# Optimization experiments

Hardware: AMD Instinct MI355X
Metric: run time of the kernel (lower is better)

## Reference

```python
import jax, jax.numpy as jnp
import numpy as np

B_SZ, L_SEQ = 8, 4096
D_MODEL, D_CONV, D_MAMBA = 512, 256, 256
DSTATE, N_HEADS, K, FFN = 64, 4, 3, 2048
EPS = 1e-6


def setup_inputs() -> dict:
    key = jax.random.key(0)
    ks = jax.random.split(key, 14)
    def rn(k, shape, scale=0.02):
        return jax.random.normal(k, shape, jnp.float32) * scale
    return {
        "x": rn(ks[0], (B_SZ, L_SEQ, D_MODEL), 1.0),
        "velocity": rn(ks[1], (B_SZ, L_SEQ, D_MODEL), 0.1),
        "pre_norm_w": jnp.ones((D_MODEL,), jnp.float32),
        "conv_in_w": rn(ks[2], (D_MODEL, 2 * D_CONV)),
        "conv_dw_w": rn(ks[3], (D_CONV, K), 0.1),
        "conv_dw_b": jnp.zeros((D_CONV,), jnp.float32),
        "x_proj_w": rn(ks[4], (D_MODEL, D_MAMBA)),
        "dt_w": rn(ks[5], (D_MODEL, D_MAMBA), 0.001),
        "dt_b": jnp.full((D_MAMBA,), -4.0, jnp.float32),
        "B_w": rn(ks[6], (D_MODEL, DSTATE)),
        "C_w": rn(ks[7], (D_MODEL, DSTATE)),
        "A_log": jnp.tile(jnp.log(jnp.arange(1, DSTATE + 1, dtype=jnp.float32))[None, :], (N_HEADS, 1)),
        "D": jnp.ones((D_MAMBA,), jnp.float32),
        "ssm_out_w": rn(ks[8], (D_MAMBA, D_MAMBA)),
        "out_proj_w": rn(ks[9], (D_MODEL, D_MODEL)),
        "log_beta": jnp.asarray(0.0, jnp.float32),  # sigmoid(0)=0.5 = beta_init
        "ffn_norm_w": jnp.ones((D_MODEL,), jnp.float32),
        "w1": rn(ks[10], (D_MODEL, FFN)),
        "w3": rn(ks[11], (D_MODEL, FFN)),
        "w2": rn(ks[12], (FFN, D_MODEL)),
    }


def _rmsnorm(x, w):
    xf = x.astype(jnp.float32)
    r = jax.lax.rsqrt(jnp.mean(xf * xf, axis=-1, keepdims=True) + EPS)
    return (xf * r).astype(x.dtype) * w


def _gated_conv(xn, conv_in_w, conv_dw_w, conv_dw_b):
    # project to 2*d_conv, causal depthwise conv on first half, silu-gate with second half
    uv = xn @ conv_in_w                       # [B,L,2*dc]
    u, g = uv[..., :D_CONV], uv[..., D_CONV:]
    up = jnp.pad(u, ((0, 0), (K - 1, 0), (0, 0)))
    L = xn.shape[1]
    conv = conv_dw_b
    for k in range(K):                        # tiny fixed kernel loop
        conv = conv + up[:, k:k + L, :] * conv_dw_w[:, k]
    return conv * jax.nn.silu(g)              # [B,L,d_conv]


def _ssm(xn, x_proj_w, dt_w, dt_b, B_w, C_w, A_log, D, ssm_out_w):
    x_ssm = xn @ x_proj_w                                     # [B,L,dm]
    dt_raw = jnp.clip(xn @ dt_w + dt_b, -10.0, 5.0)
    dt = jnp.clip(jax.nn.softplus(dt_raw), 1e-4, 0.1)         # [B,L,dm]
    Bm = xn @ B_w                                             # [B,L,ds]
    Cm = xn @ C_w
    Bm = Bm / jnp.clip(jnp.linalg.norm(Bm, axis=-1, keepdims=True), 1.0)
    Cm = Cm / jnp.clip(jnp.linalg.norm(Cm, axis=-1, keepdims=True), 1.0)
    A = -jnp.exp(A_log.reshape(-1))                           # [dm], channel c -> head c//ds, state c%ds
    Bfull = jnp.tile(Bm, (1, 1, N_HEADS))                     # [B,L,dm]: B[..., c % ds]
    Cfull = jnp.tile(Cm, (1, 1, N_HEADS))
    decay = jnp.exp(dt * A)                                   # [B,L,dm]
    inp = dt * Bfull * x_ssm

    def step(h, di):
        d_, i_ = di
        h = d_ * h + i_
        return h, h

    h0 = jnp.zeros((xn.shape[0], D_MAMBA), x_ssm.dtype)
    _, hs = jax.lax.scan(step, h0, (jnp.swapaxes(decay, 0, 1), jnp.swapaxes(inp, 0, 1)))
    y = jnp.swapaxes(hs, 0, 1) * Cfull + D * x_ssm            # [B,L,dm]
    return y @ ssm_out_w


def reference(x, velocity, pre_norm_w, conv_in_w, conv_dw_w, conv_dw_b,
              x_proj_w, dt_w, dt_b, B_w, C_w, A_log, D, ssm_out_w,
              out_proj_w, log_beta, ffn_norm_w, w1, w3, w2):
    xn = _rmsnorm(x, pre_norm_w)
    conv_out = _gated_conv(xn, conv_in_w, conv_dw_w, conv_dw_b)
    ssm_out = _ssm(xn, x_proj_w, dt_w, dt_b, B_w, C_w, A_log, D, ssm_out_w)
    mixer = jnp.concatenate([conv_out, ssm_out], axis=-1) @ out_proj_w
    beta = jax.nn.sigmoid(log_beta)
    velocity = beta * velocity + mixer
    x = x + velocity
    # fused manual RMSNorm (fp32) + SwiGLU + residual
    xf = x.astype(jnp.float32)
    rms = jax.lax.rsqrt(jnp.mean(xf * xf, axis=-1, keepdims=True) + EPS)
    normed = (xf * rms).astype(x.dtype) * ffn_norm_w
    ffn = (jax.nn.silu(normed @ w1) * (normed @ w3)) @ w2
    x = x + ffn
    return (x, velocity)
```

## Files before the change

### kernel.cpp

```cpp
#include <hip/hip_runtime.h>

#define MTOK   32768
#define LSEQ   4096
#define BSZ    8
#define DM     512
#define DC     256
#define DMAMBA 256
#define DST    64
#define NPROJ  1152
#define FFN_D  2048
#define NCH    64
#define CLEN   64

typedef __attribute__((ext_vector_type(4))) float          f32x4;
typedef __attribute__((ext_vector_type(8))) unsigned short u16x8;
typedef __attribute__((ext_vector_type(8))) __bf16         bf16x8;

typedef const __attribute__((address_space(1))) unsigned int* gptr_t;
typedef __attribute__((address_space(3))) unsigned int*       lptr_t;

static __device__ __forceinline__ unsigned short f2bf(float f) {
    unsigned int u = __builtin_bit_cast(unsigned int, f);
    u += 0x7fffu + ((u >> 16) & 1u);
    return (unsigned short)(u >> 16);
}

static __device__ __forceinline__ float wred(float s) {
#pragma unroll
    for (int m = 1; m < 64; m <<= 1) s += __shfl_xor(s, m);
    return s;
}

static __device__ __forceinline__ f32x4 mfma16(u16x8 a, u16x8 b, f32x4 c) {
    return __builtin_amdgcn_mfma_f32_16x16x32_bf16(
        __builtin_bit_cast(bf16x8, a), __builtin_bit_cast(bf16x8, b), c, 0, 0, 0);
}

static __device__ __forceinline__ void gl16(const unsigned short* g, unsigned short* l) {
    __builtin_amdgcn_global_load_lds((gptr_t)g, (lptr_t)l, 16, 0, 0);
}

template <int EPI>
__global__ __launch_bounds__(256) void gemm_nt(
    const unsigned short* __restrict__ A, const unsigned short* __restrict__ Bt,
    const unsigned short* __restrict__ B2t, void* __restrict__ Cp,
    const float* __restrict__ Cin, int K, int ldc)
{
    __shared__ unsigned short As[2 * 128 * 32];
    __shared__ unsigned short Bs[2 * 128 * 32];
    __shared__ unsigned short Bs2[(EPI == 2) ? 2 * 128 * 32 : 8];

    const int tid = threadIdx.x;
    const int lane = tid & 63, wid = tid >> 6;
    const int wr = wid >> 1, wc = wid & 1;
    const long n0 = (long)blockIdx.x * 128;
    const long m0 = (long)blockIdx.y * 128;

    f32x4 acc[4][4], acc2[4][4];
#pragma unroll
    for (int i = 0; i < 4; i++)
#pragma unroll
        for (int j = 0; j < 4; j++) {
            acc[i][j] = f32x4{0.f, 0.f, 0.f, 0.f};
            acc2[i][j] = f32x4{0.f, 0.f, 0.f, 0.f};
        }

    const int srow = wid * 32 + (lane >> 2);
    const int scol = (lane & 3) * 8;
    const unsigned short* agp = A + (m0 + srow) * (long)K + scol;
    const unsigned short* bgp = Bt + (n0 + srow) * (long)K + scol;
    const unsigned short* b2gp = (EPI == 2) ? (B2t + (n0 + srow) * (long)K + scol) : nullptr;
    const long skip = 16 * (long)K;

    const int fr = lane & 15, fo = (lane >> 4) * 8;

    auto STAGE = [&](int buf, int k0) {
        unsigned short* dA = As + buf * 4096 + wid * 1024;
        unsigned short* dB = Bs + buf * 4096 + wid * 1024;
        gl16(agp + k0, dA);
        gl16(agp + k0 + skip, dA + 512);
        gl16(bgp + k0, dB);
        gl16(bgp + k0 + skip, dB + 512);
        if constexpr (EPI == 2) {
            unsigned short* dB2 = Bs2 + buf * 4096 + wid * 1024;
            gl16(b2gp + k0, dB2);
            gl16(b2gp + k0 + skip, dB2 + 512);
        }
    };

    auto COMPUTE = [&](int buf) {
        const unsigned short* sA = As + buf * 4096;
        const unsigned short* sB = Bs + buf * 4096;
        u16x8 av[4], bv[4], cv[4];
#pragma unroll
        for (int i = 0; i < 4; i++)
            av[i] = *(const u16x8*)(sA + (wr * 64 + i * 16 + fr) * 32 + fo);
#pragma unroll
        for (int j = 0; j < 4; j++)
            bv[j] = *(const u16x8*)(sB + (wc * 64 + j * 16 + fr) * 32 + fo);
        if constexpr (EPI == 2) {
            const unsigned short* sB2 = Bs2 + buf * 4096;
#pragma unroll
            for (int j = 0; j < 4; j++)
                cv[j] = *(const u16x8*)(sB2 + (wc * 64 + j * 16 + fr) * 32 + fo);
        }
#pragma unroll
        for (int i = 0; i < 4; i++)
#pragma unroll
            for (int j = 0; j < 4; j++) {
                acc[i][j] = mfma16(av[i], bv[j], acc[i][j]);
                if constexpr (EPI == 2) acc2[i][j] = mfma16(av[i], cv[j], acc2[i][j]);
            }
    };

    STAGE(0, 0);
    __syncthreads();
    int cur = 0;
    for (int k0 = 32; k0 < K; k0 += 32) {
        STAGE(cur ^ 1, k0);
        COMPUTE(cur);
        __syncthreads();
        cur ^= 1;
    }
    COMPUTE(cur);

    const int frow = (lane >> 4) * 4;
#pragma unroll
    for (int i = 0; i < 4; i++)
#pragma unroll
        for (int j = 0; j < 4; j++)
#pragma unroll
            for (int r = 0; r < 4; r++) {
                long row = m0 + wr * 64 + i * 16 + frow + r;
                long col = n0 + wc * 64 + j * 16 + fr;
                long idx = row * (long)ldc + col;
                float v = acc[i][j][r];
                if constexpr (EPI == 0) {
                    ((float*)Cp)[idx] = v;
                } else if constexpr (EPI == 1) {
                    ((unsigned short*)Cp)[idx] = f2bf(v);
                } else if constexpr (EPI == 2) {
                    float h3 = acc2[i][j][r];
                    float s = v / (1.f + __expf(-v));
                    ((unsigned short*)Cp)[idx] = f2bf(s * h3);
                } else {
                    ((float*)Cp)[idx] = Cin[idx] + v;
                }
            }
}

struct TD { const float* s; unsigned short* d; int K, N, nb; };
struct TP { TD t[10]; };

__global__ __launch_bounds__(256) void transpose_all_k(TP p)
{
    int b = blockIdx.x;
#pragma unroll
    for (int i = 0; i < 10; i++) {
        TD td = p.t[i];
        if (b < td.nb) {
            int idx = b * 256 + threadIdx.x;
            if (idx < td.K * td.N) {
                int k = idx / td.N, n = idx - k * td.N;
                td.d[(long)n * td.K + k] = f2bf(td.s[idx]);
            }
            return;
        }
        b -= td.nb;
    }
}

__global__ __launch_bounds__(256) void rmsnorm1_k(const float* __restrict__ x,
                                                  const float* __restrict__ w,
                                                  unsigned short* __restrict__ out)
{
    const int lane = threadIdx.x & 63, wv = threadIdx.x >> 6;
    const long tok = (long)blockIdx.x * 4 + wv;
    const float* xr = x + tok * DM;
    float4 v[2];
    float s = 0.f;
#pragma unroll
    for (int j = 0; j < 2; j++) {
        int d0 = j * 256 + lane * 4;
        v[j] = *(const float4*)(xr + d0);
        s += v[j].x * v[j].x + v[j].y * v[j].y + v[j].z * v[j].z + v[j].w * v[j].w;
    }
    s = wred(s);
    float r = rsqrtf(s * (1.f / DM) + 1e-6f);
#pragma unroll
    for (int j = 0; j < 2; j++) {
        int d0 = j * 256 + lane * 4;
        const float4 ww = *(const float4*)(w + d0);
        *(ushort4*)(out + tok * DM + d0) = make_ushort4(
            f2bf(v[j].x * r * ww.x), f2bf(v[j].y * r * ww.y),
            f2bf(v[j].z * r * ww.z), f2bf(v[j].w * r * ww.w));
    }
}

__global__ __launch_bounds__(256) void mamba_prep_k(
    const float* __restrict__ proj, const float* __restrict__ dt_b,
    const float* __restrict__ A_log, const float* __restrict__ conv_w,
    const float* __restrict__ conv_b,
    float* __restrict__ decay, float* __restrict__ inp, float* __restrict__ cmn,
    unsigned short* __restrict__ mixin)
{
    const int lane = threadIdx.x & 63, wv = threadIdx.x >> 6;
    const long tok = (long)blockIdx.x * 4 + wv;
    const int l = (int)(tok & (LSEQ - 1));
    const float* pr = proj + tok * NPROJ;

    float bv = pr[1024 + lane];
    float cv = pr[1088 + lane];
    float nb2 = wred(bv * bv);
    float nc2 = wred(cv * cv);
    float rb = 1.f / fmaxf(sqrtf(nb2), 1.f);
    float rc = 1.f / fmaxf(sqrtf(nc2), 1.f);
    float bn = bv * rb;
    cmn[tok * DST + lane] = cv * rc;

#pragma unroll
    for (int j = 0; j < 4; j++) {
        int d = j * 64 + lane;
        float dtr = pr[768 + d] + dt_b[d];
        dtr = fminf(fmaxf(dtr, -10.f), 5.f);
        float sp = log1pf(__expf(dtr));
        float dt = fminf(fmaxf(sp, 1e-4f), 0.1f);
        float a = -__expf(A_log[d]);
        decay[tok * DMAMBA + d] = __expf(dt * a);
        inp[tok * DMAMBA + d] = dt * bn * pr[512 + d];

        float ul  = pr[d];
        float um1 = (l >= 1) ? pr[d - NPROJ] : 0.f;
        float um2 = (l >= 2) ? pr[d - 2 * NPROJ] : 0.f;
        float conv = conv_b[d] + um2 * conv_w[d * 3] + um1 * conv_w[d * 3 + 1] + ul * conv_w[d * 3 + 2];
        float g = pr[256 + d];
        float sg = g / (1.f + __expf(-g));
        mixin[tok * DM + d] = f2bf(conv * sg);
    }
}

__global__ __launch_bounds__(256) void scan_chunk_k(const float* __restrict__ decay,
                                                    const float* __restrict__ inp,
                                                    float* __restrict__ P, float* __restrict__ S)
{
    const int bc = blockIdx.x;
    const int b = bc >> 6, c = bc & 63;
    const int d = threadIdx.x;
    long base = ((long)b * LSEQ + (long)c * CLEN) * DMAMBA + d;
    float h = 0.f, p = 1.f;
    for (int t = 0; t < CLEN; t++) {
        float dec = decay[base + (long)t * DMAMBA];
        float iv = inp[base + (long)t * DMAMBA];
        h = dec * h + iv;
        p *= dec;
    }
    P[(long)bc * DMAMBA + d] = p;
    S[(long)bc * DMAMBA + d] = h;
}

__global__ __launch_bounds__(256) void scan_prefix_k(const float* __restrict__ P,
                                                     const float* __restrict__ S,
                                                     float* __restrict__ carry)
{
    const int b = blockIdx.x, d = threadIdx.x;
    float H = 0.f;
    for (int c = 0; c < NCH; c++) {
        long i = ((long)b * NCH + c) * DMAMBA + d;
        carry[i] = H;
        H = P[i] * H + S[i];
    }
}

__global__ __launch_bounds__(256) void scan_finish_k(
    const float* __restrict__ decay, const float* __restrict__ inp,
    const float* __restrict__ carry, const float* __restrict__ cmn,
    const float* __restrict__ Dw, const float* __restrict__ proj,
    unsigned short* __restrict__ y)
{
    const int bc = blockIdx.x;
    const int b = bc >> 6, c = bc & 63;
    const int d = threadIdx.x;
    const long tok0 = (long)b * LSEQ + (long)c * CLEN;
    float h = carry[(long)bc * DMAMBA + d];
    const float dv = Dw[d];
    for (int t = 0; t < CLEN; t++) {
        long tok = tok0 + t;
        long idx = tok * DMAMBA + d;
        h = decay[idx] * h + inp[idx];
        float yv = h * cmn[tok * DST + (d & 63)] + dv * proj[tok * NPROJ + 512 + d];
        y[idx] = f2bf(yv);
    }
}

__global__ __launch_bounds__(256) void update_norm_k(
    const float* __restrict__ x, const float* __restrict__ vel,
    const float* __restrict__ mixer, const float* __restrict__ lbeta,
    const float* __restrict__ fw, float* __restrict__ outX,
    float* __restrict__ outV, unsigned short* __restrict__ normed)
{
    const int lane = threadIdx.x & 63, wv = threadIdx.x >> 6;
    const long tok = (long)blockIdx.x * 4 + wv;
    const float beta = 1.f / (1.f + __expf(-lbeta[0]));
    float xs[8];
    float s = 0.f;
#pragma unroll
    for (int j = 0; j < 2; j++) {
        const int d0 = j * 256 + lane * 4;
        const float4 xv = *(const float4*)(x + tok * DM + d0);
        const float4 vv = *(const float4*)(vel + tok * DM + d0);
        const float4 mv = *(const float4*)(mixer + tok * DM + d0);
        float4 vn, xn;
        vn.x = beta * vv.x + mv.x; xn.x = xv.x + vn.x;
        vn.y = beta * vv.y + mv.y; xn.y = xv.y + vn.y;
        vn.z = beta * vv.z + mv.z; xn.z = xv.z + vn.z;
        vn.w = beta * vv.w + mv.w; xn.w = xv.w + vn.w;
        *(float4*)(outV + tok * DM + d0) = vn;
        *(float4*)(outX + tok * DM + d0) = xn;
        s += xn.x * xn.x + xn.y * xn.y + xn.z * xn.z + xn.w * xn.w;
        xs[j * 4 + 0] = xn.x; xs[j * 4 + 1] = xn.y; xs[j * 4 + 2] = xn.z; xs[j * 4 + 3] = xn.w;
    }
    s = wred(s);
    const float r = rsqrtf(s * (1.f / DM) + 1e-6f);
#pragma unroll
    for (int j = 0; j < 2; j++) {
        const int d0 = j * 256 + lane * 4;
        const float4 ww = *(const float4*)(fw + d0);
        *(ushort4*)(normed + tok * DM + d0) = make_ushort4(
            f2bf(xs[j * 4 + 0] * r * ww.x), f2bf(xs[j * 4 + 1] * r * ww.y),
            f2bf(xs[j * 4 + 2] * r * ww.z), f2bf(xs[j * 4 + 3] * r * ww.w));
    }
}

extern "C" void kernel_launch(void* const* d_in, const int* in_sizes, int n_in,
                              void* d_out, int out_size, void* d_ws, size_t ws_size,
                              hipStream_t stream)
{
    (void)in_sizes; (void)n_in; (void)out_size; (void)ws_size;

    const float* x          = (const float*)d_in[0];
    const float* velocity   = (const float*)d_in[1];
    const float* pre_norm_w = (const float*)d_in[2];
    const float* conv_in_w  = (const float*)d_in[3];
    const float* conv_dw_w  = (const float*)d_in[4];
    const float* conv_dw_b  = (const float*)d_in[5];
    const float* x_proj_w   = (const float*)d_in[6];
    const float* dt_w       = (const float*)d_in[7];
    const float* dt_b       = (const float*)d_in[8];
    const float* B_w        = (const float*)d_in[9];
    const float* C_w        = (const float*)d_in[10];
    const float* A_log      = (const float*)d_in[11];
    const float* Dw         = (const float*)d_in[12];
    const float* ssm_out_w  = (const float*)d_in[13];
    const float* out_proj_w = (const float*)d_in[14];
    const float* log_beta   = (const float*)d_in[15];
    const float* ffn_norm_w = (const float*)d_in[16];
    const float* w1         = (const float*)d_in[17];
    const float* w3         = (const float*)d_in[18];
    const float* w2         = (const float*)d_in[19];

    char* base = (char*)d_ws;
    size_t off = 0;
    auto take = [&](size_t bytes) -> void* {
        void* p = base + off;
        off = (off + bytes + 255) & ~(size_t)255;
        return p;
    };
    unsigned short* WCAT  = (unsigned short*)take((size_t)NPROJ * DM * 2);
    unsigned short* SSMT  = (unsigned short*)take((size_t)DMAMBA * DMAMBA * 2);
    unsigned short* OUTPT = (unsigned short*)take((size_t)DM * DM * 2);
    unsigned short* W1T   = (unsigned short*)take((size_t)FFN_D * DM * 2);
    unsigned short* W3T   = (unsigned short*)take((size_t)FFN_D * DM * 2);
    unsigned short* W2T   = (unsigned short*)take((size_t)DM * FFN_D * 2);
    unsigned short* XN    = (unsigned short*)take((size_t)MTOK * DM * 2);
    float* PROJ  = (float*)take((size_t)MTOK * NPROJ * 4);
    float* DECAY = (float*)take((size_t)MTOK * DMAMBA * 4);
    float* INP   = (float*)take((size_t)MTOK * DMAMBA * 4);
    float* CMN   = (float*)take((size_t)MTOK * DST * 4);
    float* PP    = (float*)take((size_t)BSZ * NCH * DMAMBA * 4);
    float* SS    = (float*)take((size_t)BSZ * NCH * DMAMBA * 4);
    float* CARRY = (float*)take((size_t)BSZ * NCH * DMAMBA * 4);
    unsigned short* Y      = (unsigned short*)take((size_t)MTOK * DMAMBA * 2);
    unsigned short* MIXIN  = (unsigned short*)take((size_t)MTOK * DM * 2);
    unsigned short* NORMED = (unsigned short*)take((size_t)MTOK * DM * 2);
    float* MIXER = DECAY;
    unsigned short* ACT = XN;
    float* outX = (float*)d_out;
    float* outV = outX + (size_t)MTOK * DM;

    TP tp;
    int tblk = 0;
    auto addT = [&](int i, const float* s, unsigned short* dst, int K, int N) {
        int nb = (K * N + 255) / 256;
        tp.t[i] = TD{s, dst, K, N, nb};
        tblk += nb;
    };
    addT(0, conv_in_w, WCAT, DM, DM);
    addT(1, x_proj_w, WCAT + 512 * DM, DM, DMAMBA);
    addT(2, dt_w, WCAT + 768 * DM, DM, DMAMBA);
    addT(3, B_w, WCAT + 1024 * DM, DM, DST);
    addT(4, C_w, WCAT + 1088 * DM, DM, DST);
    addT(5, ssm_out_w, SSMT, DMAMBA, DMAMBA);
    addT(6, out_proj_w, OUTPT, DM, DM);
    addT(7, w1, W1T, DM, FFN_D);
    addT(8, w3, W3T, DM, FFN_D);
    addT(9, w2, W2T, FFN_D, DM);
    transpose_all_k<<<tblk, 256, 0, stream>>>(tp);

    rmsnorm1_k<<<MTOK / 4, 256, 0, stream>>>(x, pre_norm_w, XN);

    gemm_nt<0><<<dim3(NPROJ / 128, MTOK / 128), 256, 0, stream>>>(
        XN, WCAT, nullptr, PROJ, nullptr, DM, NPROJ);

    mamba_prep_k<<<MTOK / 4, 256, 0, stream>>>(PROJ, dt_b, A_log, conv_dw_w, conv_dw_b,
                                               DECAY, INP, CMN, MIXIN);

    scan_chunk_k<<<BSZ * NCH, 256, 0, stream>>>(DECAY, INP, PP, SS);
    scan_prefix_k<<<BSZ, 256, 0, stream>>>(PP, SS, CARRY);
    scan_finish_k<<<BSZ * NCH, 256, 0, stream>>>(DECAY, INP, CARRY, CMN, Dw, PROJ, Y);

    gemm_nt<1><<<dim3(DMAMBA / 128, MTOK / 128), 256, 0, stream>>>(
        Y, SSMT, nullptr, (void*)(MIXIN + 256), nullptr, DMAMBA, DM);

    gemm_nt<0><<<dim3(DM / 128, MTOK / 128), 256, 0, stream>>>(
        MIXIN, OUTPT, nullptr, MIXER, nullptr, DM, DM);

    update_norm_k<<<MTOK / 4, 256, 0, stream>>>(x, velocity, MIXER, log_beta, ffn_norm_w,
                                                outX, outV, NORMED);

    gemm_nt<2><<<dim3(FFN_D / 128, MTOK / 128), 256, 0, stream>>>(
        NORMED, W1T, W3T, ACT, nullptr, DM, FFN_D);

    gemm_nt<3><<<dim3(DM / 128, MTOK / 128), 256, 0, stream>>>(
        ACT, W2T, nullptr, (void*)outX, (const float*)outX, FFN_D, DM);
}
```

Measured before the change: 883.6 us.

## Add 256x256 pipelined GEMM kernel with swizzled LDS and split SwiGLU GEMM

Adds a 512-thread GEMM with 256x256 tiles, K-step 64, XOR-swizzled LDS, explicit vmcnt waits and s_setprio around the MFMA blocks. It replaces the projection, out-projection, FFN and down-projection GEMMs. The projection width is padded to 1280 with zeroed weight rows so it divides the tile size. The fused w1/w3 dual-accumulator GEMM is split into two passes, with H1 stored as bf16 and combined in the second epilogue. This trades extra traffic and one more launch for larger tiles, more reuse per block and better load/compute overlap.

```diff
diff --git a/kernel.cpp b/kernel.cpp
--- a/kernel.cpp
+++ b/kernel.cpp
@@ -8,6 +8,7 @@
 #define DMAMBA 256
 #define DST    64
 #define NPROJ  1152
+#define NPROJP 1280
 #define FFN_D  2048
 #define NCH    64
 #define CLEN   64
@@ -40,15 +41,152 @@
     __builtin_amdgcn_global_load_lds((gptr_t)g, (lptr_t)l, 16, 0, 0);
 }
 
+#define VMCNT4 asm volatile("s_waitcnt vmcnt(4)" ::: "memory")
+#define VMCNT0 asm volatile("s_waitcnt vmcnt(0)" ::: "memory")
+#define LGKM0  do { asm volatile("s_waitcnt lgkmcnt(0)" ::: "memory"); \
+                    __builtin_amdgcn_sched_barrier(0); } while (0)
+
+template <int EPI>
+__global__ __launch_bounds__(512) void gemm256(
+    const unsigned short* __restrict__ A, const unsigned short* __restrict__ Bt,
+    const unsigned short* __restrict__ aux, void* __restrict__ Cp,
+    const float* __restrict__ Cin, int K, int ldc)
+{
+    __shared__ unsigned short As[2 * 256 * 64];
+    __shared__ unsigned short Bs[2 * 256 * 64];
+
+    const int tid = threadIdx.x;
+    const int lane = tid & 63, wid = tid >> 6;
+    const int wr = wid >> 2, wcol = wid & 3;
+    const long n0 = (long)blockIdx.x * 256;
+    const long m0 = (long)blockIdx.y * 256;
+    const int NT = K >> 6;
+
+    f32x4 acc[8][4];
+#pragma unroll
+    for (int i = 0; i < 8; i++)
+#pragma unroll
+        for (int j = 0; j < 4; j++) acc[i][j] = f32x4{0.f, 0.f, 0.f, 0.f};
+
+    const int sr = lane >> 3;
+    const int scol = ((lane & 7) ^ (lane >> 3)) * 8;
+
+    auto stageA = [&](int k0, int half, int sl) {
+#pragma unroll
+        for (int qq = 0; qq < 2; qq++) {
+            int c = wid * 2 + qq;
+            const unsigned short* src = A + (m0 + half * 128 + c * 8 + sr) * (long)K + k0 + scol;
+            gl16(src, As + sl * 16384 + half * 8192 + c * 512);
+        }
+    };
+    auto stageB = [&](int k0, int half, int sl) {
+#pragma unroll
+        for (int qq = 0; qq < 2; qq++) {
+            int c = wid * 2 + qq;
+            const unsigned short* src = Bt + (n0 + half * 128 + c * 8 + sr) * (long)K + k0 + scol;
+            gl16(src, Bs + sl * 16384 + half * 8192 + c * 512);
+        }
+    };
+
+    const int fr = lane & 15;
+    const int cB0 = (lane >> 4) * 16;
+    auto ldA = [&](int sl, int row, int cb) -> u16x8 {
+        int off = row * 128 + cb;
+        off ^= (row & 7) << 4;
+        return *(const u16x8*)((const char*)As + sl * 32768 + off);
+    };
+    auto ldB = [&](int sl, int row, int cb) -> u16x8 {
+        int off = row * 128 + cb;
+        off ^= (row & 7) << 4;
+        return *(const u16x8*)((const char*)Bs + sl * 32768 + off);
+    };
+
+    stageA(0, 0, 0); stageA(0, 1, 0);
+    stageB(0, 0, 0); stageB(0, 1, 0);
+    if (NT > 1) { stageB(64, 0, 1); stageB(64, 1, 1); VMCNT4; }
+    else VMCNT0;
+    __builtin_amdgcn_s_barrier();
+
+    int slot = 0;
+    for (int t = 0; t < NT; ++t) {
+        const int kN = (t + 1) << 6;
+        const int kN2 = (t + 2) << 6;
+        u16x8 bv[4][2];
+#pragma unroll
+        for (int q = 0; q < 4; q++) {
+            u16x8 av[2][2];
+#pragma unroll
+            for (int ii = 0; ii < 2; ii++) {
+                int row = wr * 128 + (q * 2 + ii) * 16 + fr;
+                av[ii][0] = ldA(slot, row, cB0);
+                av[ii][1] = ldA(slot, row, 64 + cB0);
+            }
+            if (q == 0) {
+#pragma unroll
+                for (int j = 0; j < 4; j++) {
+                    int row = wcol * 64 + j * 16 + fr;
+                    bv[j][0] = ldB(slot, row, cB0);
+                    bv[j][1] = ldB(slot, row, 64 + cB0);
+                }
+            }
+            if (q == 0 && t + 1 < NT) stageA(kN, 0, slot ^ 1);
+            if (q == 1 && t + 1 < NT) stageA(kN, 1, slot ^ 1);
+            if (q == 2 && t + 2 < NT) stageB(kN2, 0, slot);
+            if (q == 3 && t + 2 < NT) stageB(kN2, 1, slot);
+
+            __builtin_amdgcn_s_barrier();
+            LGKM0;
+            __builtin_amdgcn_s_setprio(1);
+#pragma unroll
+            for (int ii = 0; ii < 2; ii++)
+#pragma unroll
+                for (int j = 0; j < 4; j++) {
+                    acc[q * 2 + ii][j] = mfma16(av[ii][0], bv[j][0], acc[q * 2 + ii][j]);
+                    acc[q * 2 + ii][j] = mfma16(av[ii][1], bv[j][1], acc[q * 2 + ii][j]);
+                }
+            __builtin_amdgcn_s_setprio(0);
+            if (q == 3 && t + 1 < NT) {
+                if (t + 2 < NT) VMCNT4;
+                else VMCNT0;
+            }
+            __builtin_amdgcn_s_barrier();
+        }
+        slot ^= 1;
+    }
+
+    const int frow = (lane >> 4) * 4;
+#pragma unroll
+    for (int i = 0; i < 8; i++)
+#pragma unroll
+        for (int j = 0; j < 4; j++)
+#pragma unroll
+            for (int r = 0; r < 4; r++) {
+                long row = m0 + wr * 128 + i * 16 + frow + r;
+                long col = n0 + wcol * 64 + j * 16 + fr;
+                long idx = row * (long)ldc + col;
+                float v = acc[i][j][r];
+                if constexpr (EPI == 0) {
+                    ((float*)Cp)[idx] = v;
+                } else if constexpr (EPI == 1) {
+                    ((unsigned short*)Cp)[idx] = f2bf(v);
+                } else if constexpr (EPI == 2) {
+                    unsigned int u = (unsigned int)((const unsigned short*)aux)[idx] << 16;
+                    float h = __builtin_bit_cast(float, u);
+                    float s = h / (1.f + __expf(-h));
+                    ((unsigned short*)Cp)[idx] = f2bf(s * v);
+                } else {
+                    ((float*)Cp)[idx] = Cin[idx] + v;
+                }
+            }
+}
+
 template <int EPI>
 __global__ __launch_bounds__(256) void gemm_nt(
     const unsigned short* __restrict__ A, const unsigned short* __restrict__ Bt,
-    const unsigned short* __restrict__ B2t, void* __restrict__ Cp,
-    const float* __restrict__ Cin, int K, int ldc)
+    void* __restrict__ Cp, int K, int ldc)
 {
     __shared__ unsigned short As[2 * 128 * 32];
     __shared__ unsigned short Bs[2 * 128 * 32];
-    __shared__ unsigned short Bs2[(EPI == 2) ? 2 * 128 * 32 : 8];
 
     const int tid = threadIdx.x;
     const int lane = tid & 63, wid = tid >> 6;
@@ -56,22 +194,17 @@
     const long n0 = (long)blockIdx.x * 128;
     const long m0 = (long)blockIdx.y * 128;
 
-    f32x4 acc[4][4], acc2[4][4];
+    f32x4 acc[4][4];
 #pragma unroll
     for (int i = 0; i < 4; i++)
 #pragma unroll
-        for (int j = 0; j < 4; j++) {
-            acc[i][j] = f32x4{0.f, 0.f, 0.f, 0.f};
-            acc2[i][j] = f32x4{0.f, 0.f, 0.f, 0.f};
-        }
+        for (int j = 0; j < 4; j++) acc[i][j] = f32x4{0.f, 0.f, 0.f, 0.f};
 
     const int srow = wid * 32 + (lane >> 2);
     const int scol = (lane & 3) * 8;
     const unsigned short* agp = A + (m0 + srow) * (long)K + scol;
     const unsigned short* bgp = Bt + (n0 + srow) * (long)K + scol;
-    const unsigned short* b2gp = (EPI == 2) ? (B2t + (n0 + srow) * (long)K + scol) : nullptr;
     const long skip = 16 * (long)K;
-
     const int fr = lane & 15, fo = (lane >> 4) * 8;
 
     auto STAGE = [&](int buf, int k0) {
@@ -81,36 +214,22 @@
         gl16(agp + k0 + skip, dA + 512);
         gl16(bgp + k0, dB);
         gl16(bgp + k0 + skip, dB + 512);
-        if constexpr (EPI == 2) {
-            unsigned short* dB2 = Bs2 + buf * 4096 + wid * 1024;
-            gl16(b2gp + k0, dB2);
-            gl16(b2gp + k0 + skip, dB2 + 512);
-        }
-    };
-
+    };
     auto COMPUTE = [&](int buf) {
         const unsigned short* sA = As + buf * 4096;
         const unsigned short* sB = Bs + buf * 4096;
-        u16x8 av[4], bv[4], cv[4];
+        u16x8 av[4], bv[4];
 #pragma unroll
         for (int i = 0; i < 4; i++)
             av[i] = *(const u16x8*)(sA + (wr * 64 + i * 16 + fr) * 32 + fo);
 #pragma unroll
         for (int j = 0; j < 4; j++)
             bv[j] = *(const u16x8*)(sB + (wc * 64 + j * 16 + fr) * 32 + fo);
-        if constexpr (EPI == 2) {
-            const unsigned short* sB2 = Bs2 + buf * 4096;
+#pragma unroll
+        for (int i = 0; i < 4; i++)
 #pragma unroll
             for (int j = 0; j < 4; j++)
-                cv[j] = *(const u16x8*)(sB2 + (wc * 64 + j * 16 + fr) * 32 + fo);
-        }
-#pragma unroll
-        for (int i = 0; i < 4; i++)
-#pragma unroll
-            for (int j = 0; j < 4; j++) {
                 acc[i][j] = mfma16(av[i], bv[j], acc[i][j]);
-                if constexpr (EPI == 2) acc2[i][j] = mfma16(av[i], cv[j], acc2[i][j]);
-            }
     };
 
     STAGE(0, 0);
@@ -134,35 +253,28 @@
                 long row = m0 + wr * 64 + i * 16 + frow + r;
                 long col = n0 + wc * 64 + j * 16 + fr;
                 long idx = row * (long)ldc + col;
-                float v = acc[i][j][r];
-                if constexpr (EPI == 0) {
-                    ((float*)Cp)[idx] = v;
-                } else if constexpr (EPI == 1) {
-                    ((unsigned short*)Cp)[idx] = f2bf(v);
-                } else if constexpr (EPI == 2) {
-                    float h3 = acc2[i][j][r];
-                    float s = v / (1.f + __expf(-v));
-                    ((unsigned short*)Cp)[idx] = f2bf(s * h3);
-                } else {
-                    ((float*)Cp)[idx] = Cin[idx] + v;
-                }
+                ((unsigned short*)Cp)[idx] = f2bf(acc[i][j][r]);
             }
 }
 
 struct TD { const float* s; unsigned short* d; int K, N, nb; };
-struct TP { TD t[10]; };
+struct TP { TD t[11]; };
 
 __global__ __launch_bounds__(256) void transpose_all_k(TP p)
 {
     int b = blockIdx.x;
 #pragma unroll
-    for (int i = 0; i < 10; i++) {
+    for (int i = 0; i < 11; i++) {
         TD td = p.t[i];
         if (b < td.nb) {
             int idx = b * 256 + threadIdx.x;
             if (idx < td.K * td.N) {
-                int k = idx / td.N, n = idx - k * td.N;
-                td.d[(long)n * td.K + k] = f2bf(td.s[idx]);
+                if (td.s == nullptr) {
+                    td.d[idx] = 0;
+                } else {
+                    int k = idx / td.N, n = idx - k * td.N;
+                    td.d[(long)n * td.K + k] = f2bf(td.s[idx]);
+                }
             }
             return;
         }
@@ -207,7 +319,7 @@
     const int lane = threadIdx.x & 63, wv = threadIdx.x >> 6;
     const long tok = (long)blockIdx.x * 4 + wv;
     const int l = (int)(tok & (LSEQ - 1));
-    const float* pr = proj + tok * NPROJ;
+    const float* pr = proj + tok * NPROJP;
 
     float bv = pr[1024 + lane];
     float cv = pr[1088 + lane];
@@ -230,8 +342,8 @@
         inp[tok * DMAMBA + d] = dt * bn * pr[512 + d];
 
         float ul  = pr[d];
-        float um1 = (l >= 1) ? pr[d - NPROJ] : 0.f;
-        float um2 = (l >= 2) ? pr[d - 2 * NPROJ] : 0.f;
+        float um1 = (l >= 1) ? pr[d - NPROJP] : 0.f;
+        float um2 = (l >= 2) ? pr[d - 2 * NPROJP] : 0.f;
         float conv = conv_b[d] + um2 * conv_w[d * 3] + um1 * conv_w[d * 3 + 1] + ul * conv_w[d * 3 + 2];
         float g = pr[256 + d];
         float sg = g / (1.f + __expf(-g));
@@ -287,7 +399,7 @@
         long tok = tok0 + t;
         long idx = tok * DMAMBA + d;
         h = decay[idx] * h + inp[idx];
-        float yv = h * cmn[tok * DST + (d & 63)] + dv * proj[tok * NPROJ + 512 + d];
+        float yv = h * cmn[tok * DST + (d & 63)] + dv * proj[tok * NPROJP + 512 + d];
         y[idx] = f2bf(yv);
     }
 }
@@ -365,14 +477,14 @@
         off = (off + bytes + 255) & ~(size_t)255;
         return p;
     };
-    unsigned short* WCAT  = (unsigned short*)take((size_t)NPROJ * DM * 2);
+    unsigned short* WCAT  = (unsigned short*)take((size_t)NPROJP * DM * 2);
     unsigned short* SSMT  = (unsigned short*)take((size_t)DMAMBA * DMAMBA * 2);
     unsigned short* OUTPT = (unsigned short*)take((size_t)DM * DM * 2);
     unsigned short* W1T   = (unsigned short*)take((size_t)FFN_D * DM * 2);
     unsigned short* W3T   = (unsigned short*)take((size_t)FFN_D * DM * 2);
     unsigned short* W2T   = (unsigned short*)take((size_t)DM * FFN_D * 2);
     unsigned short* XN    = (unsigned short*)take((size_t)MTOK * DM * 2);
-    float* PROJ  = (float*)take((size_t)MTOK * NPROJ * 4);
+    float* PROJ  = (float*)take((size_t)MTOK * NPROJP * 4);
     float* DECAY = (float*)take((size_t)MTOK * DMAMBA * 4);
     float* INP   = (float*)take((size_t)MTOK * DMAMBA * 4);
     float* CMN   = (float*)take((size_t)MTOK * DST * 4);
@@ -384,6 +496,7 @@
     unsigned short* NORMED = (unsigned short*)take((size_t)MTOK * DM * 2);
     float* MIXER = DECAY;
     unsigned short* ACT = XN;
+    unsigned short* H1  = (unsigned short*)PROJ;
     float* outX = (float*)d_out;
     float* outV = outX + (size_t)MTOK * DM;
 
@@ -404,12 +517,13 @@
     addT(7, w1, W1T, DM, FFN_D);
     addT(8, w3, W3T, DM, FFN_D);
     addT(9, w2, W2T, FFN_D, DM);
+    addT(10, nullptr, WCAT + 1152 * DM, 128, DM);
     transpose_all_k<<<tblk, 256, 0, stream>>>(tp);
 
     rmsnorm1_k<<<MTOK / 4, 256, 0, stream>>>(x, pre_norm_w, XN);
 
-    gemm_nt<0><<<dim3(NPROJ / 128, MTOK / 128), 256, 0, stream>>>(
-        XN, WCAT, nullptr, PROJ, nullptr, DM, NPROJ);
+    gemm256<0><<<dim3(NPROJP / 256, MTOK / 256), 512, 0, stream>>>(
+        XN, WCAT, nullptr, PROJ, nullptr, DM, NPROJP);
 
     mamba_prep_k<<<MTOK / 4, 256, 0, stream>>>(PROJ, dt_b, A_log, conv_dw_w, conv_dw_b,
                                                DECAY, INP, CMN, MIXIN);
@@ -419,17 +533,20 @@
     scan_finish_k<<<BSZ * NCH, 256, 0, stream>>>(DECAY, INP, CARRY, CMN, Dw, PROJ, Y);
 
     gemm_nt<1><<<dim3(DMAMBA / 128, MTOK / 128), 256, 0, stream>>>(
-        Y, SSMT, nullptr, (void*)(MIXIN + 256), nullptr, DMAMBA, DM);
-
-    gemm_nt<0><<<dim3(DM / 128, MTOK / 128), 256, 0, stream>>>(
+        Y, SSMT, (void*)(MIXIN + 256), DMAMBA, DM);
+
+    gemm256<0><<<dim3(DM / 256, MTOK / 256), 512, 0, stream>>>(
         MIXIN, OUTPT, nullptr, MIXER, nullptr, DM, DM);
 
     update_norm_k<<<MTOK / 4, 256, 0, stream>>>(x, velocity, MIXER, log_beta, ffn_norm_w,
                                                 outX, outV, NORMED);
 
-    gemm_nt<2><<<dim3(FFN_D / 128, MTOK / 128), 256, 0, stream>>>(
-        NORMED, W1T, W3T, ACT, nullptr, DM, FFN_D);
-
-    gemm_nt<3><<<dim3(DM / 128, MTOK / 128), 256, 0, stream>>>(
+    gemm256<1><<<dim3(FFN_D / 256, MTOK / 256), 512, 0, stream>>>(
+        NORMED, W1T, nullptr, H1, nullptr, DM, FFN_D);
+
+    gemm256<2><<<dim3(FFN_D / 256, MTOK / 256), 512, 0, stream>>>(
+        NORMED, W3T, H1, ACT, nullptr, DM, FFN_D);
+
+    gemm256<3><<<dim3(DM / 256, MTOK / 256), 512, 0, stream>>>(
         ACT, W2T, nullptr, (void*)outX, (const float*)outX, FFN_D, DM);
 }
```

Measured after the change: 827.4 us. -6.4%, faster.
